# Optimization experiments

Hardware: AMD Instinct MI355X
Metric: run time of the kernel (lower is better)

The kernel has to match this reference:

```python
import jax, jax.numpy as jnp
import numpy as np

L, D, H, M = 4, 256, 8, 1024  # num_blocks, emb_dim, num_heads, mlp_dim
B, N = 8, 1024
HD = H * D  # per-head dim == emb_dim in this module (hidden_dims = emb_dim*num_heads)


def setup_inputs() -> dict:
    key = jax.random.key(0)
    ks = jax.random.split(key, 6)
    s = 0.02
    return {
        "x": jax.random.normal(ks[0], (B, N, D), jnp.float32),
        "ln1_g": jnp.ones((L, D), jnp.float32),
        "ln1_b": jnp.zeros((L, D), jnp.float32),
        "qkv_w": jax.random.normal(ks[1], (L, D, 3 * HD), jnp.float32) * s,
        "qkv_b": jnp.zeros((L, 3 * HD), jnp.float32),
        "proj_w": jax.random.normal(ks[2], (L, HD, D), jnp.float32) * s,
        "proj_b": jnp.zeros((L, D), jnp.float32),
        "ln2_g": jnp.ones((L, D), jnp.float32),
        "ln2_b": jnp.zeros((L, D), jnp.float32),
        "w1": jax.random.normal(ks[3], (L, D, M), jnp.float32) * s,
        "b1": jnp.zeros((L, M), jnp.float32),
        "w2": jax.random.normal(ks[4], (L, M, D), jnp.float32) * s,
        "b2": jnp.zeros((L, D), jnp.float32),
    }


def _layernorm(x, g, b):
    m = x.mean(-1, keepdims=True)
    v = x.var(-1, keepdims=True)  # torch LayerNorm: biased variance, eps=1e-5
    return (x - m) * jax.lax.rsqrt(v + 1e-5) * g + b


def reference(x, ln1_g, ln1_b, qkv_w, qkv_b, proj_w, proj_b, ln2_g, ln2_b, w1, b1, w2, b2):
    b, n, d = x.shape
    scale = d ** 0.5  # source intends emb_dim**0.5; NOTE: applied AFTER softmax (bug preserved)
    for i in range(L):
        # --- attention residual block (pre-norm) ---
        h = _layernorm(x, ln1_g[i], ln1_b[i])
        qkv = (h @ qkv_w[i] + qkv_b[i]).reshape(b, n, H, d, 3)  # 'b n (h d qkv)'
        q = jnp.transpose(qkv[..., 0], (0, 2, 1, 3))  # [b,H,n,d]
        k = jnp.transpose(qkv[..., 1], (0, 2, 1, 3))
        v = jnp.transpose(qkv[..., 2], (0, 2, 1, 3))
        energy = jnp.einsum('bhqd,bhkd->bhqk', q, k)
        attn = jax.nn.softmax(energy, axis=-1) / scale  # post-softmax scaling as in source
        o = jnp.einsum('bhal,bhlv->bhav', attn, v)
        o = jnp.transpose(o, (0, 2, 1, 3)).reshape(b, n, H * d)
        x = x + (o @ proj_w[i] + proj_b[i])
        # --- MLP residual block (pre-norm) ---
        h = _layernorm(x, ln2_g[i], ln2_b[i])
        h = jax.nn.gelu(h @ w1[i] + b1[i], approximate=False)  # torch nn.GELU default = exact
        x = x + (h @ w2[i] + b2[i])
    return x
```

## Files before the change

kernel.cpp:

```cpp
#include <hip/hip_runtime.h>
#include <cstdint>
#include <cmath>

typedef float f32x4 __attribute__((ext_vector_type(4)));
typedef short s16x8 __attribute__((ext_vector_type(8)));

__device__ __forceinline__ unsigned short f2bf(float f) {
  union { float f; unsigned u; } v; v.f = f;
  unsigned r = v.u + 0x7FFFu + ((v.u >> 16) & 1u);
  return (unsigned short)(r >> 16);
}

__device__ __forceinline__ void async16(const void* g, void* l) {
  __builtin_amdgcn_global_load_lds(
      (const __attribute__((address_space(1))) unsigned int*)g,
      (__attribute__((address_space(3))) unsigned int*)l, 16, 0, 0);
}

#define MFMA(a,b,c) __builtin_amdgcn_mfma_f32_16x16x32_bf16((a),(b),(c),0,0,0)

#define Lb 4
#define Dm 256
#define Hh 8
#define Mm 1024
#define Bb 8
#define Nn 1024
#define ROWS (Bb*Nn)
#define QKVN (3*Hh*Dm)

__global__ __launch_bounds__(256) void ln_kernel(const float* __restrict__ x,
                                                 const float* __restrict__ g,
                                                 const float* __restrict__ b,
                                                 unsigned short* __restrict__ out) {
  int wave = threadIdx.x >> 6, lane = threadIdx.x & 63;
  int row = blockIdx.x * 4 + wave;
  const float4* xr = (const float4*)(x + (size_t)row * Dm);
  float4 v = xr[lane];
  float s = v.x + v.y + v.z + v.w;
  float s2 = v.x*v.x + v.y*v.y + v.z*v.z + v.w*v.w;
  #pragma unroll
  for (int off = 1; off < 64; off <<= 1) {
    s  += __shfl_xor(s,  off);
    s2 += __shfl_xor(s2, off);
  }
  float mean = s * (1.0f/Dm);
  float var  = s2 * (1.0f/Dm) - mean*mean;
  float inv  = rsqrtf(var + 1e-5f);
  float4 gg = ((const float4*)g)[lane];
  float4 bb = ((const float4*)b)[lane];
  ushort4 o;
  o.x = f2bf((v.x-mean)*inv*gg.x + bb.x);
  o.y = f2bf((v.y-mean)*inv*gg.y + bb.y);
  o.z = f2bf((v.z-mean)*inv*gg.z + bb.z);
  o.w = f2bf((v.w-mean)*inv*gg.w + bb.w);
  ((ushort4*)(out + (size_t)row * Dm))[lane] = o;
}

__global__ __launch_bounds__(256) void lncomb_kernel(const float* __restrict__ xin,
                                                     const float* __restrict__ pp, int nz,
                                                     const float* __restrict__ g,
                                                     const float* __restrict__ b,
                                                     float* __restrict__ xout,
                                                     unsigned short* __restrict__ hb) {
  int wave = threadIdx.x >> 6, lane = threadIdx.x & 63;
  int row = blockIdx.x * 4 + wave;
  size_t base = (size_t)row * Dm;
  float4 v = ((const float4*)(xin + base))[lane];
  #pragma unroll 4
  for (int z = 0; z < nz; z++) {
    float4 p = ((const float4*)(pp + (size_t)z * ROWS * Dm + base))[lane];
    v.x += p.x; v.y += p.y; v.z += p.z; v.w += p.w;
  }
  ((float4*)(xout + base))[lane] = v;
  float s = v.x + v.y + v.z + v.w;
  float s2 = v.x*v.x + v.y*v.y + v.z*v.z + v.w*v.w;
  #pragma unroll
  for (int off = 1; off < 64; off <<= 1) {
    s  += __shfl_xor(s,  off);
    s2 += __shfl_xor(s2, off);
  }
  float mean = s * (1.0f/Dm);
  float var  = s2 * (1.0f/Dm) - mean*mean;
  float inv  = rsqrtf(var + 1e-5f);
  float4 gg = ((const float4*)g)[lane];
  float4 bb = ((const float4*)b)[lane];
  ushort4 o;
  o.x = f2bf((v.x-mean)*inv*gg.x + bb.x);
  o.y = f2bf((v.y-mean)*inv*gg.y + bb.y);
  o.z = f2bf((v.z-mean)*inv*gg.z + bb.z);
  o.w = f2bf((v.w-mean)*inv*gg.w + bb.w);
  ((ushort4*)(hb + base))[lane] = o;
}

__global__ __launch_bounds__(256) void comb_out_kernel(const float* __restrict__ xin,
                                                       const float* __restrict__ pp, int nz,
                                                       float* __restrict__ out) {
  int wave = threadIdx.x >> 6, lane = threadIdx.x & 63;
  int row = blockIdx.x * 4 + wave;
  size_t base = (size_t)row * Dm;
  float4 v = ((const float4*)(xin + base))[lane];
  #pragma unroll 4
  for (int z = 0; z < nz; z++) {
    float4 p = ((const float4*)(pp + (size_t)z * ROWS * Dm + base))[lane];
    v.x += p.x; v.y += p.y; v.z += p.z; v.w += p.w;
  }
  ((float4*)(out + base))[lane] = v;
}

template<bool PERM>
__global__ __launch_bounds__(256) void convT(const float* __restrict__ w,
                                             unsigned short* __restrict__ wt,
                                             int Kd, int Nd) {
  __shared__ float tile[32][33];
  int nt = blockIdx.x * 32, kt = blockIdx.y * 32, l = blockIdx.z;
  int tx = threadIdx.x & 31, ty = threadIdx.x >> 5;
  const float* src = w + ((size_t)l * Kd + kt) * Nd + nt;
  #pragma unroll
  for (int r = 0; r < 4; r++)
    tile[ty + r*8][tx] = src[(size_t)(ty + r*8) * Nd + tx];
  __syncthreads();
  #pragma unroll
  for (int r = 0; r < 4; r++) {
    int nl = ty + r*8;
    int j = nt + nl;
    int n = j;
    if (PERM) {
      int hh = j / 768, rem = j - hh*768;
      int dd = rem / 3, c = rem - dd*3;
      n = c*2048 + hh*256 + dd;
    }
    wt[((size_t)l * Nd + n) * Kd + kt + tx] = f2bf(tile[tx][nl]);
  }
}

__global__ void conv_bias(const float* __restrict__ bsrc, float* __restrict__ bperm) {
  int i = blockIdx.x * 256 + threadIdx.x;
  int l = i / QKVN, n = i - l*QKVN;
  int c = n >> 11, hh = (n >> 8) & 7, dd = n & 255;
  bperm[i] = bsrc[l*QKVN + hh*768 + dd*3 + c];
}

template<int EPI, int BN>
__global__ __launch_bounds__(256, (BN == 128) ? 2 : 4)
void gemm_bt(const unsigned short* __restrict__ A,
             const unsigned short* __restrict__ Bt,
             const float* __restrict__ bias,
             void* __restrict__ outv,
             unsigned short* __restrict__ vtg,
             int M, int N, int Kstride, int Ksub) {
  constexpr int BM = 128, BK = 32;
  constexpr int NI = BN / 32;
  __shared__ __align__(16) unsigned short As[2][BM * BK];
  __shared__ __align__(16) unsigned short Bs[2][BN * BK];
  __shared__ __align__(16) unsigned short vtile[(EPI == 3) ? 128 * 136 : 1];
  int tid = threadIdx.x;
  int lane = tid & 63, wave = tid >> 6;
  int wm = (wave >> 1) * 64, wn = (wave & 1) * (BN / 2);
  int mblk = blockIdx.y * BM, nblk = blockIdx.x * BN;
  int l15 = lane & 15, q4 = lane >> 4;

  f32x4 acc[4][NI] = {};

  int r0 = tid >> 2;
  int ch = (tid & 3) ^ ((tid >> 3) & 3);
  const unsigned short* Ag = A + (size_t)blockIdx.z * Ksub
                               + (size_t)(mblk + r0) * Kstride + ch*8;
  const unsigned short* Bg = Bt + (size_t)blockIdx.z * Ksub
                               + (size_t)(nblk + r0) * Kstride + ch*8;

  async16(Ag,                      As[0] + tid*8);
  async16(Ag + (size_t)64*Kstride, As[0] + 2048 + tid*8);
  async16(Bg,                      Bs[0] + tid*8);
  if (BN == 128)
    async16(Bg + (size_t)64*Kstride, Bs[0] + 2048 + tid*8);

  int xsw = (q4 ^ ((l15 >> 1) & 3)) * 8;

  int nk = Ksub / BK;
  for (int i = 0; i < nk; i++) {
    __syncthreads();
    if (i + 1 < nk) {
      int k0 = (i + 1) * BK;
      unsigned short* Asl = As[(i+1)&1] + tid*8;
      unsigned short* Bsl = Bs[(i+1)&1] + tid*8;
      async16(Ag + k0,                      Asl);
      async16(Ag + (size_t)64*Kstride + k0, Asl + 2048);
      async16(Bg + k0,                      Bsl);
      if (BN == 128)
        async16(Bg + (size_t)64*Kstride + k0, Bsl + 2048);
    }
    const unsigned short* Ac = As[i&1];
    const unsigned short* Bc = Bs[i&1];
    s16x8 af[4], bf[NI];
    #pragma unroll
    for (int j = 0; j < 4; j++)
      af[j] = *(const s16x8*)(Ac + (wm + j*16 + l15) * BK + xsw);
    #pragma unroll
    for (int j = 0; j < NI; j++)
      bf[j] = *(const s16x8*)(Bc + (wn + j*16 + l15) * BK + xsw);
    #pragma unroll
    for (int mi = 0; mi < 4; mi++)
      #pragma unroll
      for (int ni = 0; ni < NI; ni++)
        acc[mi][ni] = MFMA(af[mi], bf[ni], acc[mi][ni]);
  }

  auto scalar_epi = [&]() {
    #pragma unroll
    for (int mi = 0; mi < 4; mi++)
      #pragma unroll
      for (int ni = 0; ni < NI; ni++) {
        int col = nblk + wn + ni*16 + l15;
        float bcol;
        if (EPI == 4) bcol = (blockIdx.z == 0) ? bias[col] : 0.0f;
        else          bcol = bias[col];
        #pragma unroll
        for (int r = 0; r < 4; r++) {
          int row = mblk + wm + mi*16 + q4*4 + r;
          float v = acc[mi][ni][r] + bcol;
          if (EPI == 1) {
            v = 0.5f * v * (1.0f + erff(v * 0.70710678118f));
            ((unsigned short*)outv)[(size_t)row * N + col] = f2bf(v);
          } else if (EPI == 3) {
            ((unsigned short*)outv)[(size_t)row * 4096 + col] = f2bf(v);
          } else if (EPI == 4) {
            float* out = (float*)outv + (size_t)blockIdx.z * M * N;
            out[(size_t)row * N + col] = v;
          }
        }
      }
  };

  if constexpr (EPI == 3) {
    if (nblk >= 4096) {
      #pragma unroll
      for (int mi = 0; mi < 4; mi++)
        #pragma unroll
        for (int ni = 0; ni < NI; ni++) {
          int col_l = wn + ni*16 + l15;
          float bcol = bias[nblk + col_l];
          int seq_l = wm + mi*16 + q4*4;
          ushort4 pk4;
          pk4.x = f2bf(acc[mi][ni][0] + bcol);
          pk4.y = f2bf(acc[mi][ni][1] + bcol);
          pk4.z = f2bf(acc[mi][ni][2] + bcol);
          pk4.w = f2bf(acc[mi][ni][3] + bcol);
          *(ushort4*)(vtile + col_l * 136 + seq_l) = pk4;
        }
      __syncthreads();
      int base = nblk - 4096;
      int hh = base >> 8, ddb = base & 255;
      int bi = mblk >> 10, n0 = mblk & 1023;
      unsigned short* dst = vtg + ((size_t)(bi*8 + hh) * 256 + ddb) * 1024 + n0;
      #pragma unroll
      for (int p = 0; p < 8; p++) {
        int flat = p * 2048 + tid * 8;
        int ddl = flat >> 7, ns = flat & 127;
        int4 v4 = *(const int4*)(vtile + ddl * 136 + ns);
        *(int4*)(dst + (size_t)ddl * 1024 + ns) = v4;
      }
    } else {
      scalar_epi();
    }
  } else {
    scalar_epi();
  }
}

__global__ __launch_bounds__(256, 2) void attn_kernel(const unsigned short* __restrict__ qk,
                                                      const unsigned short* __restrict__ vt,
                                                      unsigned short* __restrict__ obuf) {
  int bh = blockIdx.x;
  int b = bh >> 3, h = bh & 7;
  int qt = blockIdx.y;
  int tid = threadIdx.x, lane = tid & 63, wave = tid >> 6;
  int l15 = lane & 15, q4 = lane >> 4;

  __shared__ __align__(16) unsigned short Ks[2][32 * 256];
  __shared__ __align__(16) unsigned short Vs[2][256 * 32];

  const unsigned short* Qb  = qk + (size_t)(b * Nn) * 4096 + h * 256;
  const unsigned short* Kb  = Qb + 2048;
  const unsigned short* VTb = vt + (size_t)bh * 256 * 1024;

  int qbase = qt * 128 + wave * 32;

  s16x8 qf[2][8];
  #pragma unroll
  for (int s = 0; s < 2; s++) {
    const unsigned short* qp = Qb + (size_t)(qbase + s*16 + l15) * 4096 + q4*8;
    #pragma unroll
    for (int c = 0; c < 8; c++) qf[s][c] = *(const s16x8*)(qp + c*32);
  }

  f32x4 oacc[2][16] = {};
  float lrun[2] = {0.f, 0.f};

  int ke[4], kc_[4], ve_[4];
  #pragma unroll
  for (int ii = 0; ii < 4; ii++) {
    int s = tid + ii*256;
    ke[ii] = s * 8;
    int kyr = s >> 5, kch = (s & 31) ^ (kyr & 7);
    kc_[ii] = kyr * 4096 + kch * 8;
    int vr = s >> 2, vch = (s & 3) ^ ((s >> 3) & 3);
    ve_[ii] = vr * 1024 + vch * 8;
  }

  #pragma unroll
  for (int ii = 0; ii < 4; ii++) {
    async16(Kb + kc_[ii],  Ks[0] + ke[ii]);
    async16(VTb + ve_[ii], Vs[0] + ke[ii]);
  }

  int vsw = (q4 ^ ((l15 >> 1) & 3)) * 8;

  for (int kt = 0; kt < 32; kt++) {
    __syncthreads();
    if (kt + 1 < 32) {
      int buf = (kt + 1) & 1;
      #pragma unroll
      for (int ii = 0; ii < 4; ii++) {
        async16(Kb + (size_t)(kt+1)*32*4096 + kc_[ii], Ks[buf] + ke[ii]);
        async16(VTb + (kt+1)*32 + ve_[ii],             Vs[buf] + ke[ii]);
      }
    }
    const unsigned short* Kc = Ks[kt & 1];
    const unsigned short* Vc = Vs[kt & 1];

    f32x4 sacc[2][2] = {};
    #pragma unroll
    for (int c = 0; c < 8; c++)
      #pragma unroll
      for (int mb = 0; mb < 2; mb++) {
        s16x8 af = *(const s16x8*)(Kc + (mb*16 + l15)*256 + (((c*4 + q4) ^ (l15 & 7)))*8);
        sacc[0][mb] = MFMA(af, qf[0][c], sacc[0][mb]);
        sacc[1][mb] = MFMA(af, qf[1][c], sacc[1][mb]);
      }

    int pk[2][2][2];
    #pragma unroll
    for (int s = 0; s < 2; s++) {
      float v0[4], v1[4];
      float rs = 0.f;
      #pragma unroll
      for (int r = 0; r < 4; r++) {
        v0[r] = __expf(sacc[s][0][r] - 12.0f);
        v1[r] = __expf(sacc[s][1][r] - 12.0f);
        rs += v0[r] + v1[r];
      }
      rs += __shfl_xor(rs, 16);
      rs += __shfl_xor(rs, 32);
      lrun[s] += rs;
      pk[s][0][0] = (int)f2bf(v0[0]) | ((int)f2bf(v0[1]) << 16);
      pk[s][0][1] = (int)f2bf(v0[2]) | ((int)f2bf(v0[3]) << 16);
      pk[s][1][0] = (int)f2bf(v1[0]) | ((int)f2bf(v1[1]) << 16);
      pk[s][1][1] = (int)f2bf(v1[2]) | ((int)f2bf(v1[3]) << 16);
    }

    int src0 = l15 + 16 * ((q4 & 1) * 2);
    int src1 = src0 + 16;
    bool sel = (q4 < 2);
    s16x8 pa[2];
    #pragma unroll
    for (int s = 0; s < 2; s++) {
      int u00 = __shfl(pk[s][0][0], src0), u10 = __shfl(pk[s][1][0], src0);
      int u01 = __shfl(pk[s][0][1], src0), u11 = __shfl(pk[s][1][1], src0);
      int u02 = __shfl(pk[s][0][0], src1), u12 = __shfl(pk[s][1][0], src1);
      int u03 = __shfl(pk[s][0][1], src1), u13 = __shfl(pk[s][1][1], src1);
      union { int u[4]; s16x8 v; } P;
      P.u[0] = sel ? u00 : u10;
      P.u[1] = sel ? u01 : u11;
      P.u[2] = sel ? u02 : u12;
      P.u[3] = sel ? u03 : u13;
      pa[s] = P.v;
    }

    #pragma unroll
    for (int nb = 0; nb < 16; nb++) {
      s16x8 vf = *(const s16x8*)(Vc + (nb*16 + l15)*32 + vsw);
      oacc[0][nb] = MFMA(pa[0], vf, oacc[0][nb]);
      oacc[1][nb] = MFMA(pa[1], vf, oacc[1][nb]);
    }
  }

  #pragma unroll
  for (int s = 0; s < 2; s++) {
    float lr[4];
    #pragma unroll
    for (int r = 0; r < 4; r++) lr[r] = __shfl(lrun[s], q4*4 + r);
    #pragma unroll
    for (int r = 0; r < 4; r++) {
      float sc = 1.0f / (lr[r] * 16.0f);
      int row = b * Nn + qbase + s*16 + q4*4 + r;
      unsigned short* op = obuf + (size_t)row * 2048 + h * 256;
      #pragma unroll
      for (int nb = 0; nb < 16; nb++)
        op[nb*16 + l15] = f2bf(oacc[s][nb][r] * sc);
    }
  }
}

extern "C" void kernel_launch(void* const* d_in, const int* in_sizes, int n_in,
                              void* d_out, int out_size, void* d_ws, size_t ws_size,
                              hipStream_t stream) {
  const float* x_in   = (const float*)d_in[0];
  const float* ln1_g  = (const float*)d_in[1];
  const float* ln1_b  = (const float*)d_in[2];
  const float* qkv_w  = (const float*)d_in[3];
  const float* qkv_b  = (const float*)d_in[4];
  const float* proj_w = (const float*)d_in[5];
  const float* proj_b = (const float*)d_in[6];
  const float* ln2_g  = (const float*)d_in[7];
  const float* ln2_b  = (const float*)d_in[8];
  const float* w1     = (const float*)d_in[9];
  const float* b1     = (const float*)d_in[10];
  const float* w2     = (const float*)d_in[11];
  const float* b2     = (const float*)d_in[12];

  char* ws = (char*)d_ws;
  size_t off = 0;
  float*          X0   = (float*)(ws + off);          off += (size_t)ROWS*Dm*4;
  unsigned short* Hb   = (unsigned short*)(ws + off); off += (size_t)ROWS*Dm*2;
  char*           QKre = ws + off;                    off += (size_t)ROWS*4096*2;
  unsigned short* VT   = (unsigned short*)(ws + off); off += (size_t)64*256*1024*2;
  unsigned short* O    = (unsigned short*)(ws + off); off += (size_t)ROWS*2048*2;
  unsigned short* H1   = (unsigned short*)(ws + off); off += (size_t)ROWS*Mm*2;
  unsigned short* QKVW = (unsigned short*)(ws + off); off += (size_t)Lb*QKVN*Dm*2;
  float*          QKVB = (float*)(ws + off);          off += (size_t)Lb*QKVN*4;
  unsigned short* PRJW = (unsigned short*)(ws + off); off += (size_t)Lb*Dm*2048*2;
  unsigned short* W1T  = (unsigned short*)(ws + off); off += (size_t)Lb*Mm*Dm*2;
  unsigned short* W2T  = (unsigned short*)(ws + off); off += (size_t)Lb*Dm*Mm*2;

  unsigned short* QK = (unsigned short*)QKre;
  float*          PP = (float*)QKre;
  float*          X1 = (float*)(QKre + (size_t)36*1024*1024);

  hipMemcpyAsync(X0, x_in, (size_t)ROWS*Dm*4, hipMemcpyDeviceToDevice, stream);

  convT<true><<<dim3(QKVN/32, Dm/32, Lb), 256, 0, stream>>>(qkv_w, QKVW, Dm, QKVN);
  conv_bias<<<Lb*QKVN/256, 256, 0, stream>>>(qkv_b, QKVB);
  convT<false><<<dim3(Dm/32, 2048/32, Lb), 256, 0, stream>>>(proj_w, PRJW, 2048, Dm);
  convT<false><<<dim3(Mm/32, Dm/32, Lb), 256, 0, stream>>>(w1, W1T, Dm, Mm);
  convT<false><<<dim3(Dm/32, Mm/32, Lb), 256, 0, stream>>>(w2, W2T, Mm, Dm);

  for (int l = 0; l < Lb; l++) {
    if (l == 0)
      ln_kernel<<<ROWS/4, 256, 0, stream>>>(X0, ln1_g, ln1_b, Hb);
    gemm_bt<3,128><<<dim3(QKVN/128, ROWS/128), 256, 0, stream>>>(
        Hb, QKVW + (size_t)l*QKVN*Dm, QKVB + (size_t)l*QKVN, QK, VT,
        ROWS, QKVN, Dm, Dm);
    attn_kernel<<<dim3(Bb*Hh, Nn/128), 256, 0, stream>>>(QK, VT, O);
    gemm_bt<4,64><<<dim3(Dm/64, ROWS/128, 4), 256, 0, stream>>>(
        O, PRJW + (size_t)l*Dm*2048, proj_b + l*Dm, PP, nullptr,
        ROWS, Dm, 2048, 512);
    lncomb_kernel<<<ROWS/4, 256, 0, stream>>>(X0, PP, 4, ln2_g + l*Dm, ln2_b + l*Dm,
                                              X1, Hb);
    gemm_bt<1,64><<<dim3(Mm/64, ROWS/128), 256, 0, stream>>>(
        Hb, W1T + (size_t)l*Mm*Dm, b1 + l*Mm, H1, nullptr, ROWS, Mm, Dm, Dm);
    gemm_bt<4,64><<<dim3(Dm/64, ROWS/128, 4), 256, 0, stream>>>(
        H1, W2T + (size_t)l*Dm*Mm, b2 + l*Dm, PP, nullptr,
        ROWS, Dm, Mm, 256);
    if (l < Lb - 1) {
      lncomb_kernel<<<ROWS/4, 256, 0, stream>>>(X1, PP, 4, ln1_g + (l+1)*Dm,
                                                ln1_b + (l+1)*Dm, X0, Hb);
    } else {
      comb_out_kernel<<<ROWS/4, 256, 0, stream>>>(X1, PP, 4, (float*)d_out);
    }
  }
}
```

Measured before the change: 960.4 us.

## Templatize GEMM tile shape, split V-transpose epilogue, use truncating bf16 pack

Makes the GEMM M-tile a template parameter and switches the proj, MLP1 and MLP2 GEMMs from 128x64 to 64x128 tiles. Occupancy for the 128-row tile rises from 2 to 3 blocks per CU. The QKV V-transpose epilogue now writes through a half-size LDS tile in two passes, cutting shared memory use so three blocks fit. In attention, P is packed to bf16 by truncation instead of round-to-nearest, which saves ALU work but adds a small precision loss.

```diff
diff --git a/kernel.cpp b/kernel.cpp
--- a/kernel.cpp
+++ b/kernel.cpp
@@ -9,6 +9,11 @@
   union { float f; unsigned u; } v; v.f = f;
   unsigned r = v.u + 0x7FFFu + ((v.u >> 16) & 1u);
   return (unsigned short)(r >> 16);
+}
+
+__device__ __forceinline__ int pk2(float a, float b) {
+  union { float f; unsigned u; } x, y; x.f = a; y.f = b;
+  return (int)((x.u >> 16) | (y.u & 0xFFFF0000u));
 }
 
 __device__ __forceinline__ void async16(const void* g, void* l) {
@@ -140,26 +145,27 @@
   bperm[i] = bsrc[l*QKVN + hh*768 + dd*3 + c];
 }
 
-template<int EPI, int BN>
-__global__ __launch_bounds__(256, (BN == 128) ? 2 : 4)
+template<int EPI, int BM, int BN>
+__global__ __launch_bounds__(256, (BM == 128) ? 3 : 4)
 void gemm_bt(const unsigned short* __restrict__ A,
              const unsigned short* __restrict__ Bt,
              const float* __restrict__ bias,
              void* __restrict__ outv,
              unsigned short* __restrict__ vtg,
              int M, int N, int Kstride, int Ksub) {
-  constexpr int BM = 128, BK = 32;
-  constexpr int NI = BN / 32;
+  constexpr int BK = 32;
+  constexpr int MI = BM / 32, NI = BN / 32;
+  constexpr int AST = BM / 64, BST = BN / 64;
   __shared__ __align__(16) unsigned short As[2][BM * BK];
   __shared__ __align__(16) unsigned short Bs[2][BN * BK];
-  __shared__ __align__(16) unsigned short vtile[(EPI == 3) ? 128 * 136 : 1];
+  __shared__ __align__(16) unsigned short vtile[(EPI == 3) ? 128 * 68 : 1];
   int tid = threadIdx.x;
   int lane = tid & 63, wave = tid >> 6;
-  int wm = (wave >> 1) * 64, wn = (wave & 1) * (BN / 2);
+  int wm = (wave >> 1) * (BM / 2), wn = (wave & 1) * (BN / 2);
   int mblk = blockIdx.y * BM, nblk = blockIdx.x * BN;
   int l15 = lane & 15, q4 = lane >> 4;
 
-  f32x4 acc[4][NI] = {};
+  f32x4 acc[MI][NI] = {};
 
   int r0 = tid >> 2;
   int ch = (tid & 3) ^ ((tid >> 3) & 3);
@@ -168,11 +174,10 @@
   const unsigned short* Bg = Bt + (size_t)blockIdx.z * Ksub
                                + (size_t)(nblk + r0) * Kstride + ch*8;
 
-  async16(Ag,                      As[0] + tid*8);
-  async16(Ag + (size_t)64*Kstride, As[0] + 2048 + tid*8);
-  async16(Bg,                      Bs[0] + tid*8);
-  if (BN == 128)
-    async16(Bg + (size_t)64*Kstride, Bs[0] + 2048 + tid*8);
+  #pragma unroll
+  for (int t = 0; t < AST; t++) async16(Ag + (size_t)t*64*Kstride, As[0] + t*2048 + tid*8);
+  #pragma unroll
+  for (int t = 0; t < BST; t++) async16(Bg + (size_t)t*64*Kstride, Bs[0] + t*2048 + tid*8);
 
   int xsw = (q4 ^ ((l15 >> 1) & 3)) * 8;
 
@@ -183,23 +188,22 @@
       int k0 = (i + 1) * BK;
       unsigned short* Asl = As[(i+1)&1] + tid*8;
       unsigned short* Bsl = Bs[(i+1)&1] + tid*8;
-      async16(Ag + k0,                      Asl);
-      async16(Ag + (size_t)64*Kstride + k0, Asl + 2048);
-      async16(Bg + k0,                      Bsl);
-      if (BN == 128)
-        async16(Bg + (size_t)64*Kstride + k0, Bsl + 2048);
+      #pragma unroll
+      for (int t = 0; t < AST; t++) async16(Ag + (size_t)t*64*Kstride + k0, Asl + t*2048);
+      #pragma unroll
+      for (int t = 0; t < BST; t++) async16(Bg + (size_t)t*64*Kstride + k0, Bsl + t*2048);
     }
     const unsigned short* Ac = As[i&1];
     const unsigned short* Bc = Bs[i&1];
-    s16x8 af[4], bf[NI];
-    #pragma unroll
-    for (int j = 0; j < 4; j++)
+    s16x8 af[MI], bf[NI];
+    #pragma unroll
+    for (int j = 0; j < MI; j++)
       af[j] = *(const s16x8*)(Ac + (wm + j*16 + l15) * BK + xsw);
     #pragma unroll
     for (int j = 0; j < NI; j++)
       bf[j] = *(const s16x8*)(Bc + (wn + j*16 + l15) * BK + xsw);
     #pragma unroll
-    for (int mi = 0; mi < 4; mi++)
+    for (int mi = 0; mi < MI; mi++)
       #pragma unroll
       for (int ni = 0; ni < NI; ni++)
         acc[mi][ni] = MFMA(af[mi], bf[ni], acc[mi][ni]);
@@ -207,7 +211,7 @@
 
   auto scalar_epi = [&]() {
     #pragma unroll
-    for (int mi = 0; mi < 4; mi++)
+    for (int mi = 0; mi < MI; mi++)
       #pragma unroll
       for (int ni = 0; ni < NI; ni++) {
         int col = nblk + wn + ni*16 + l15;
@@ -233,31 +237,37 @@
 
   if constexpr (EPI == 3) {
     if (nblk >= 4096) {
-      #pragma unroll
-      for (int mi = 0; mi < 4; mi++)
-        #pragma unroll
-        for (int ni = 0; ni < NI; ni++) {
-          int col_l = wn + ni*16 + l15;
-          float bcol = bias[nblk + col_l];
-          int seq_l = wm + mi*16 + q4*4;
-          ushort4 pk4;
-          pk4.x = f2bf(acc[mi][ni][0] + bcol);
-          pk4.y = f2bf(acc[mi][ni][1] + bcol);
-          pk4.z = f2bf(acc[mi][ni][2] + bcol);
-          pk4.w = f2bf(acc[mi][ni][3] + bcol);
-          *(ushort4*)(vtile + col_l * 136 + seq_l) = pk4;
-        }
-      __syncthreads();
       int base = nblk - 4096;
       int hh = base >> 8, ddb = base & 255;
       int bi = mblk >> 10, n0 = mblk & 1023;
       unsigned short* dst = vtg + ((size_t)(bi*8 + hh) * 256 + ddb) * 1024 + n0;
       #pragma unroll
-      for (int p = 0; p < 8; p++) {
-        int flat = p * 2048 + tid * 8;
-        int ddl = flat >> 7, ns = flat & 127;
-        int4 v4 = *(const int4*)(vtile + ddl * 136 + ns);
-        *(int4*)(dst + (size_t)ddl * 1024 + ns) = v4;
+      for (int half = 0; half < 2; half++) {
+        if (half) __syncthreads();
+        if ((wm >> 6) == half) {
+          #pragma unroll
+          for (int mi = 0; mi < MI; mi++)
+            #pragma unroll
+            for (int ni = 0; ni < NI; ni++) {
+              int col_l = wn + ni*16 + l15;
+              float bcol = bias[nblk + col_l];
+              int seq_l = mi*16 + q4*4;
+              ushort4 pk4;
+              pk4.x = f2bf(acc[mi][ni][0] + bcol);
+              pk4.y = f2bf(acc[mi][ni][1] + bcol);
+              pk4.z = f2bf(acc[mi][ni][2] + bcol);
+              pk4.w = f2bf(acc[mi][ni][3] + bcol);
+              *(ushort4*)(vtile + col_l * 68 + seq_l) = pk4;
+            }
+        }
+        __syncthreads();
+        #pragma unroll
+        for (int p = 0; p < 4; p++) {
+          int flat = p * 2048 + tid * 8;
+          int ddl = flat >> 6, ns = flat & 63;
+          int4 v4 = *(const int4*)(vtile + ddl * 68 + ns);
+          *(int4*)(dst + (size_t)ddl * 1024 + half*64 + ns) = v4;
+        }
       }
     } else {
       scalar_epi();
@@ -352,10 +362,10 @@
       rs += __shfl_xor(rs, 16);
       rs += __shfl_xor(rs, 32);
       lrun[s] += rs;
-      pk[s][0][0] = (int)f2bf(v0[0]) | ((int)f2bf(v0[1]) << 16);
-      pk[s][0][1] = (int)f2bf(v0[2]) | ((int)f2bf(v0[3]) << 16);
-      pk[s][1][0] = (int)f2bf(v1[0]) | ((int)f2bf(v1[1]) << 16);
-      pk[s][1][1] = (int)f2bf(v1[2]) | ((int)f2bf(v1[3]) << 16);
+      pk[s][0][0] = pk2(v0[0], v0[1]);
+      pk[s][0][1] = pk2(v0[2], v0[3]);
+      pk[s][1][0] = pk2(v1[0], v1[1]);
+      pk[s][1][1] = pk2(v1[2], v1[3]);
     }
 
     int src0 = l15 + 16 * ((q4 & 1) * 2);
@@ -447,18 +457,18 @@
   for (int l = 0; l < Lb; l++) {
     if (l == 0)
       ln_kernel<<<ROWS/4, 256, 0, stream>>>(X0, ln1_g, ln1_b, Hb);
-    gemm_bt<3,128><<<dim3(QKVN/128, ROWS/128), 256, 0, stream>>>(
+    gemm_bt<3,128,128><<<dim3(QKVN/128, ROWS/128), 256, 0, stream>>>(
         Hb, QKVW + (size_t)l*QKVN*Dm, QKVB + (size_t)l*QKVN, QK, VT,
         ROWS, QKVN, Dm, Dm);
     attn_kernel<<<dim3(Bb*Hh, Nn/128), 256, 0, stream>>>(QK, VT, O);
-    gemm_bt<4,64><<<dim3(Dm/64, ROWS/128, 4), 256, 0, stream>>>(
+    gemm_bt<4,64,128><<<dim3(Dm/128, ROWS/64, 4), 256, 0, stream>>>(
         O, PRJW + (size_t)l*Dm*2048, proj_b + l*Dm, PP, nullptr,
         ROWS, Dm, 2048, 512);
     lncomb_kernel<<<ROWS/4, 256, 0, stream>>>(X0, PP, 4, ln2_g + l*Dm, ln2_b + l*Dm,
                                               X1, Hb);
-    gemm_bt<1,64><<<dim3(Mm/64, ROWS/128), 256, 0, stream>>>(
+    gemm_bt<1,64,128><<<dim3(Mm/128, ROWS/64), 256, 0, stream>>>(
         Hb, W1T + (size_t)l*Mm*Dm, b1 + l*Mm, H1, nullptr, ROWS, Mm, Dm, Dm);
-    gemm_bt<4,64><<<dim3(Dm/64, ROWS/128, 4), 256, 0, stream>>>(
+    gemm_bt<4,64,128><<<dim3(Dm/128, ROWS/64, 4), 256, 0, stream>>>(
         H1, W2T + (size_t)l*Dm*Mm, b2 + l*Dm, PP, nullptr,
         ROWS, Dm, Mm, 256);
     if (l < Lb - 1) {
```

Result: faster. 914.0 us (median of 2 runs) (-4.8%).
